# Kernel optimization log

Hardware: AMD Instinct MI355X
Metric: run time of the kernel (lower is better)

The kernel has to match this reference:

```python
import jax, jax.numpy as jnp
import numpy as np

R = 2          # candidate_radius
TEMP = 0.1     # temperature
MIN_E = 3
MAX_E = 8      # max_edges_per_node
EPS = 1e-6


def _neighbors(H, W, r):
    # grid neighbor indices (N,K) and relative positions (K,2), clamped at borders
    ys, xs = np.meshgrid(np.arange(H), np.arange(W), indexing='ij')
    idx_grid = ys * W + xs
    nbrs, rel = [], []
    for dy in range(-r, r + 1):
        for dx in range(-r, r + 1):
            if dy == 0 and dx == 0:
                continue
            ny = np.clip(ys + dy, 0, H - 1)
            nx = np.clip(xs + dx, 0, W - 1)
            nbrs.append(idx_grid[ny, nx].ravel())
            rel.append([dx / r, dy / r])
    return jnp.asarray(np.stack(nbrs, 1)), jnp.asarray(np.array(rel, np.float32))


def setup_inputs() -> dict:
    key = jax.random.key(0)
    ks = jax.random.split(key, 12)
    B, C, H, W = 2, 64, 128, 128
    hid = 64
    ein = 2 * C + 2  # edge scorer input dim
    s = 0.05
    return {
        'x':  jax.random.normal(ks[0], (B, C, H, W), jnp.float32),
        'W1': jax.random.normal(ks[1], (hid, ein), jnp.float32) * s,
        'b1': jnp.zeros((hid,), jnp.float32),
        'W2': jax.random.normal(ks[2], (hid // 2, hid), jnp.float32) * s,
        'b2': jnp.zeros((hid // 2,), jnp.float32),
        'W3': jax.random.normal(ks[3], (1, hid // 2), jnp.float32) * s,
        'b3': jnp.zeros((1,), jnp.float32),
        'thr': jnp.asarray(0.0, jnp.float32),
        'Wm': jax.random.normal(ks[4], (C, C), jnp.float32) * s,
        'bm': jnp.zeros((C,), jnp.float32),
        'Wo': jax.random.normal(ks[5], (C, C), jnp.float32) * s,
        'bo': jnp.zeros((C,), jnp.float32),
    }


def reference(x, W1, b1, W2, b2, W3, b3, thr, Wm, bm, Wo, bo):
    B, C, H, W = x.shape
    N = H * W
    nbr, rel = _neighbors(H, W, R)          # (N,K), (K,2)
    K = nbr.shape[1]

    nodes = x.transpose(0, 2, 3, 1).reshape(B, N, C)   # (B,N,C)
    h_tgt = jnp.take(nodes, nbr, axis=1)               # (B,N,K,C) gather neighbors

    # edge scorer layer1: split W1 over [h_src | h_tgt | rel_pos] to avoid (B,N,K,2C+2) concat
    z_src = nodes @ W1[:, :C].T                        # (B,N,hid)
    z_tgt = h_tgt @ W1[:, C:2 * C].T                   # (B,N,K,hid)
    z_pos = rel @ W1[:, 2 * C:].T                      # (K,hid)
    h1 = jax.nn.relu(z_src[:, :, None, :] + z_tgt + z_pos[None, None] + b1)
    h2 = jax.nn.relu(h1 @ W2.T + b2)
    edge_scores = jax.nn.sigmoid((h2 @ W3.T + b3)[..., 0])   # (B,N,K)

    thr_v = jax.nn.sigmoid(thr)
    keep_prob = jax.nn.sigmoid((edge_scores - thr_v) / TEMP)
    mask_thr = edge_scores >= thr_v
    counts = mask_thr.sum(axis=2)                       # (B,N)

    def topk_mask(k):
        _, idx = jax.lax.top_k(edge_scores, k)          # (B,N,k)
        return jax.nn.one_hot(idx, K, dtype=jnp.float32).sum(-2) > 0

    m_max = topk_mask(min(MAX_E, K))
    m_min = topk_mask(min(MIN_E, K))
    use_max = (counts > MAX_E)[..., None]
    use_min = (counts < MIN_E)[..., None]
    use_t = ~use_max & ~use_min
    final_mask = (use_max & m_max) | (use_min & m_min) | (use_t & mask_thr)

    msgs = jax.nn.relu(h_tgt @ Wm.T + bm)               # (B,N,K,C)
    w = (edge_scores * keep_prob * final_mask.astype(edge_scores.dtype))[..., None]
    agg = (msgs * w).sum(axis=2) / (w.sum(axis=2) + EPS)  # (B,N,C)

    out = nodes + agg @ Wo.T + bo
    return out.reshape(B, H, W, C).transpose(0, 3, 1, 2)
```

## Files before the change

### kernel.cpp

```cpp
#include <hip/hip_runtime.h>
#include <hip/hip_bf16.h>
#include <math.h>

#define NNODES 16384
#define KE 24

typedef float f32x4 __attribute__((ext_vector_type(4)));
typedef unsigned u32x4 __attribute__((ext_vector_type(4)));
typedef __fp16 half2_t __attribute__((ext_vector_type(2)));
typedef _Float16 half8_t __attribute__((ext_vector_type(8)));

union fragcast { u32x4 u; half8_t h; half2_t h2[4]; };

__global__ __launch_bounds__(256) void precompute_k(
    const float* __restrict__ x, const float* __restrict__ W1,
    const float* __restrict__ Wm, const float* __restrict__ b1,
    const float* __restrict__ bm,
    float* __restrict__ zsrc, float* __restrict__ ztgt, float* __restrict__ msg,
    float* __restrict__ zpos)
{
    __shared__ fragcast fragA[64 * 17];
    __shared__ float otL[4][16 * 68];

    const int t = threadIdx.x;
    const int l = t & 63;
    const int lcol = l & 15;
    const int lgrp = l >> 4;
    const int w = t >> 6;
    const int mat = blockIdx.x >> 8;
    const int tile = blockIdx.x & 255;
    const int n0g = tile * 128;
    const int b = n0g >> 14;
    const int nl0 = n0g & (NNODES - 1);

    if (blockIdx.x == 0) {
        for (int idx = t; idx < KE * 64; idx += 256) {
            int k = idx >> 6, h = idx & 63;
            int kk = k + (k >= 12 ? 1 : 0);
            int q5 = (kk * 52) >> 8;
            int dy = q5 - 2, dx = kk - 5 * q5 - 2;
            zpos[idx] = W1[h * 130 + 128] * (dx * 0.5f)
                      + W1[h * 130 + 129] * (dy * 0.5f);
        }
    }

    {
        const int mt = w;
        const int h = mt * 16 + lcol;
        const float* wrow = (mat == 0) ? (W1 + (size_t)h * 130)
                          : (mat == 1) ? (W1 + (size_t)h * 130 + 64)
                                       : (Wm + (size_t)h * 64);
        #pragma unroll
        for (int kt = 0; kt < 2; ++kt) {
            const float* wr = wrow + kt * 32 + lgrp * 8;
            fragcast fh, fl;
            #pragma unroll
            for (int d = 0; d < 4; ++d) {
                float e0 = wr[2 * d] * 64.f;
                float e1 = wr[2 * d + 1] * 64.f;
                half2_t hh = __builtin_amdgcn_cvt_pkrtz(e0, e1);
                fh.h2[d] = hh;
                fl.h2[d] = __builtin_amdgcn_cvt_pkrtz(e0 - (float)hh[0],
                                                      e1 - (float)hh[1]);
            }
            fragA[l * 17 + mt * 4 + kt * 2 + 0] = fh;
            fragA[l * 17 + mt * 4 + kt * 2 + 1] = fl;
        }
    }
    __syncthreads();

    float bv[4][4];
    #pragma unroll
    for (int mt = 0; mt < 4; ++mt)
        #pragma unroll
        for (int q = 0; q < 4; ++q) {
            int h = mt * 16 + lgrp * 4 + q;
            bv[mt][q] = (mat == 0) ? b1[h] : (mat == 2) ? bm[h] : 0.f;
        }

    const fragcast* fa = &fragA[l * 17];
    const float* xb = x + (size_t)b * 64 * NNODES + nl0;
    float* dst = (mat == 0) ? zsrc : (mat == 1) ? ztgt : msg;
    float* ot = &otL[w][0];

    #pragma unroll 1
    for (int nt = 0; nt < 2; ++nt) {
        const int nloc = w * 32 + nt * 16;

        fragcast Bh[2], Bl[2];
        #pragma unroll
        for (int kt = 0; kt < 2; ++kt) {
            const float* xc = xb + (size_t)(kt * 32 + lgrp * 8) * NNODES + nloc + lcol;
            float xv[8];
            #pragma unroll
            for (int i = 0; i < 8; ++i) xv[i] = xc[(size_t)i * NNODES];
            #pragma unroll
            for (int d = 0; d < 4; ++d) {
                half2_t hh = __builtin_amdgcn_cvt_pkrtz(xv[2 * d], xv[2 * d + 1]);
                Bh[kt].h2[d] = hh;
                Bl[kt].h2[d] = __builtin_amdgcn_cvt_pkrtz(xv[2 * d] - (float)hh[0],
                                                          xv[2 * d + 1] - (float)hh[1]);
            }
        }

        #pragma unroll
        for (int mt = 0; mt < 4; ++mt) {
            f32x4 acc = {0.f, 0.f, 0.f, 0.f};
            #pragma unroll
            for (int kt = 0; kt < 2; ++kt) {
                fragcast Ah = fa[mt * 4 + kt * 2 + 0];
                fragcast Al = fa[mt * 4 + kt * 2 + 1];
                acc = __builtin_amdgcn_mfma_f32_16x16x32_f16(Ah.h, Bh[kt].h, acc, 0, 0, 0);
                acc = __builtin_amdgcn_mfma_f32_16x16x32_f16(Al.h, Bh[kt].h, acc, 0, 0, 0);
                acc = __builtin_amdgcn_mfma_f32_16x16x32_f16(Ah.h, Bl[kt].h, acc, 0, 0, 0);
            }
            #pragma unroll
            for (int q = 0; q < 4; ++q) {
                float v = fmaf(acc[q], 0.015625f, bv[mt][q]);
                if (mat == 2) v = fmaxf(v, 0.f);
                ot[lcol * 68 + mt * 16 + lgrp * 4 + q] = v;
            }
        }

        {
            int nn = l >> 2, qt = l & 3;
            float* gout = dst + (size_t)(n0g + nloc + nn) * 64 + qt * 16;
            #pragma unroll
            for (int j = 0; j < 4; ++j) {
                f32x4 vv = *(const f32x4*)&ot[nn * 68 + qt * 16 + j * 4];
                *(float4*)(gout + j * 4) = make_float4(vv[0], vv[1], vv[2], vv[3]);
            }
        }
    }
}

__global__ __launch_bounds__(256, 1) void score_k(
    const float* __restrict__ zsrc, const float* __restrict__ ztgt,
    const float* __restrict__ zpos, const float* __restrict__ W2,
    const float* __restrict__ b2, const float* __restrict__ W3,
    const float* __restrict__ b3, float* __restrict__ scores)
{
    __shared__ fragcast fraglds[64 * 13];
    __shared__ float zpl[24 * 68];

    const int t = threadIdx.x;
    const int l = t & 63;
    const int lcol = l & 15;
    const int lgrp = l >> 4;
    const int w = t >> 6;
    const int wave = blockIdx.x * 4 + w;

    #pragma unroll
    for (int r = 0; r < 6; ++r) {
        int idx = r * 256 + t;
        zpl[(idx >> 6) * 68 + (idx & 63)] = zpos[idx];
    }
    {
        const int jt = w >> 1, kt = w & 1;
        fragcast fh, fl;
        const float* wr = W2 + (size_t)(jt * 16 + lcol) * 64 + kt * 32 + lgrp * 8;
        #pragma unroll
        for (int d = 0; d < 4; ++d) {
            float e0 = wr[2 * d] * 64.f;
            float e1 = wr[2 * d + 1] * 64.f;
            half2_t hh = __builtin_amdgcn_cvt_pkrtz(e0, e1);
            float r0 = e0 - (float)hh[0];
            float r1 = e1 - (float)hh[1];
            fh.h2[d] = hh;
            fl.h2[d] = __builtin_amdgcn_cvt_pkrtz(r0, r1);
        }
        fraglds[l * 13 + 0 + jt * 2 + kt] = fh;
        fraglds[l * 13 + 4 + jt * 2 + kt] = fl;
    }
    __syncthreads();

    const fragcast* fb = &fraglds[l * 13];
    const f32x4 b2l0 = *(const f32x4*)(b2 + lgrp * 4);
    const f32x4 b2l1 = *(const f32x4*)(b2 + 16 + lgrp * 4);
    const f32x4 w3l0 = *(const f32x4*)(W3 + lgrp * 4);
    const f32x4 w3l1 = *(const f32x4*)(W3 + 16 + lgrp * 4);
    const float b3s = b3[0];

    const int node0 = wave * 2;

    int kArr[3];
    float4 zsv[3][4], ztv[3][4];
    #pragma unroll
    for (int Mt = 0; Mt < 3; ++Mt) {
        const int ke = Mt * 16 + lcol;
        const int nsel = (ke >= 24) ? 1 : 0;
        const int node = node0 + nsel;
        const int k = ke - 24 * nsel;
        const int bb = node >> 14;
        const int nl = node & (NNODES - 1);
        const int yy = nl >> 7, xx = nl & 127;
        const int kk = k + (k >= 12 ? 1 : 0);
        const int q5 = (kk * 52) >> 8;
        const int dy = q5 - 2, dx = kk - 5 * q5 - 2;
        const int ny = min(max(yy + dy, 0), 127);
        const int nx = min(max(xx + dx, 0), 127);
        const int nbn = (bb << 14) + (ny << 7) + nx;
        kArr[Mt] = k;
        const float* zs = zsrc + (size_t)node * 64 + lgrp * 8;
        const float* zt = ztgt + (size_t)nbn * 64 + lgrp * 8;
        zsv[Mt][0] = *(const float4*)(zs);
        zsv[Mt][1] = *(const float4*)(zs + 4);
        zsv[Mt][2] = *(const float4*)(zs + 32);
        zsv[Mt][3] = *(const float4*)(zs + 36);
        ztv[Mt][0] = *(const float4*)(zt);
        ztv[Mt][1] = *(const float4*)(zt + 4);
        ztv[Mt][2] = *(const float4*)(zt + 32);
        ztv[Mt][3] = *(const float4*)(zt + 36);
    }

    #pragma unroll
    for (int Mt = 0; Mt < 3; ++Mt) {
        const float* zp = &zpl[kArr[Mt] * 68 + lgrp * 8];

        f32x4 ac0A = {0.f,0.f,0.f,0.f}, ac0B = {0.f,0.f,0.f,0.f};
        f32x4 ac1A = {0.f,0.f,0.f,0.f}, ac1B = {0.f,0.f,0.f,0.f};

        #pragma unroll
        for (int kt = 0; kt < 2; ++kt) {
            float4 a0 = zsv[Mt][2 * kt], a1 = zsv[Mt][2 * kt + 1];
            float4 t0 = ztv[Mt][2 * kt], t1 = ztv[Mt][2 * kt + 1];
            float4 p0 = *(const float4*)(zp + kt * 32);
            float4 p1 = *(const float4*)(zp + kt * 32 + 4);
            float v[8];
            v[0] = fmaxf(a0.x + t0.x + p0.x, 0.f);
            v[1] = fmaxf(a0.y + t0.y + p0.y, 0.f);
            v[2] = fmaxf(a0.z + t0.z + p0.z, 0.f);
            v[3] = fmaxf(a0.w + t0.w + p0.w, 0.f);
            v[4] = fmaxf(a1.x + t1.x + p1.x, 0.f);
            v[5] = fmaxf(a1.y + t1.y + p1.y, 0.f);
            v[6] = fmaxf(a1.z + t1.z + p1.z, 0.f);
            v[7] = fmaxf(a1.w + t1.w + p1.w, 0.f);

            fragcast Bh, Bl;
            #pragma unroll
            for (int d = 0; d < 4; ++d) {
                float e0 = v[2 * d], e1 = v[2 * d + 1];
                half2_t hh = __builtin_amdgcn_cvt_pkrtz(e0, e1);
                float r0 = e0 - (float)hh[0];
                float r1 = e1 - (float)hh[1];
                Bh.h2[d] = hh;
                Bl.h2[d] = __builtin_amdgcn_cvt_pkrtz(r0, r1);
            }

            ac0A = __builtin_amdgcn_mfma_f32_16x16x32_f16(fb[0 + kt].h, Bh.h, ac0A, 0, 0, 0);
            ac1A = __builtin_amdgcn_mfma_f32_16x16x32_f16(fb[2 + kt].h, Bh.h, ac1A, 0, 0, 0);
            ac0B = __builtin_amdgcn_mfma_f32_16x16x32_f16(fb[4 + kt].h, Bh.h, ac0B, 0, 0, 0);
            ac1B = __builtin_amdgcn_mfma_f32_16x16x32_f16(fb[6 + kt].h, Bh.h, ac1B, 0, 0, 0);
            ac0B = __builtin_amdgcn_mfma_f32_16x16x32_f16(fb[0 + kt].h, Bl.h, ac0B, 0, 0, 0);
            ac1B = __builtin_amdgcn_mfma_f32_16x16x32_f16(fb[2 + kt].h, Bl.h, ac1B, 0, 0, 0);
        }

        const f32x4 s0 = ac0A + ac0B;
        const f32x4 s1 = ac1A + ac1B;
        float sacc = 0.f;
        #pragma unroll
        for (int q = 0; q < 4; ++q) {
            sacc = fmaf(fmaxf(fmaf(s0[q], 0.015625f, b2l0[q]), 0.f), w3l0[q], sacc);
            sacc = fmaf(fmaxf(fmaf(s1[q], 0.015625f, b2l1[q]), 0.f), w3l1[q], sacc);
        }
        sacc += __shfl_xor(sacc, 16);
        sacc += __shfl_xor(sacc, 32);
        float sig = 1.f / (1.f + expf(-(sacc + b3s)));
        if (l < 16)
            scores[(size_t)node0 * 24 + Mt * 16 + l] = sig;
    }
}

__global__ __launch_bounds__(256) void agg_k(
    const float* __restrict__ x, const float* __restrict__ scores,
    const float* __restrict__ msg, const float* __restrict__ Wo,
    const float* __restrict__ bo, const float* __restrict__ thrp,
    float* __restrict__ out)
{
    __shared__ float sc[768];
    __shared__ float wl[768];
    __shared__ float sumw[32];
    __shared__ float aggL[32][64];
    __shared__ float ot[64][33];

    const int t = threadIdx.x;
    const int n0 = blockIdx.x * 32;
    const int b = n0 >> 14;
    const int nl0 = n0 & (NNODES - 1);
    const float thr_v = 1.f / (1.f + expf(-thrp[0]));

    #pragma unroll
    for (int rep = 0; rep < 3; ++rep)
        sc[rep * 256 + t] = scores[(size_t)n0 * 24 + rep * 256 + t];
    __syncthreads();

    #pragma unroll
    for (int rep = 0; rep < 3; ++rep) {
        int e = rep * 256 + t;
        int nl = (int)(((unsigned)(e >> 3) * 171u) >> 9);
        int k = e - nl * 24;
        float s_e = sc[e];
        int rank = 0, cnt = 0;
        #pragma unroll
        for (int j = 0; j < 24; ++j) {
            float sj = sc[nl * 24 + j];
            rank += (sj > s_e || (sj == s_e && j < k)) ? 1 : 0;
            cnt  += (sj >= thr_v) ? 1 : 0;
        }
        bool mask = (cnt > 8) ? (rank < 8)
                  : ((cnt < 3) ? (rank < 3) : (s_e >= thr_v));
        float keep = 1.f / (1.f + expf(-(s_e - thr_v) * 10.f));
        wl[e] = mask ? s_e * keep : 0.f;
    }
    __syncthreads();

    if (t < 32) {
        float s = 0.f;
        #pragma unroll
        for (int k = 0; k < 24; ++k) s += wl[t * 24 + k];
        sumw[t] = s + 1e-6f;
    }
    __syncthreads();

    const int lane = t & 63;
    const int g4 = t >> 6;

    #pragma unroll
    for (int it = 0; it < 8; ++it) {
        int nl = g4 + it * 4;
        int nn = nl0 + nl;
        int yy = nn >> 7, xx = nn & 127;
        float acc = 0.f;
        #pragma unroll
        for (int k = 0; k < 24; ++k) {
            int kk = k + (k >= 12 ? 1 : 0);
            int q5 = (kk * 52) >> 8;
            int dy = q5 - 2, dx = kk - 5 * q5 - 2;
            int ny = min(max(yy + dy, 0), 127);
            int nx = min(max(xx + dx, 0), 127);
            int nb = (b << 14) + (ny << 7) + nx;
            acc = fmaf(wl[nl * 24 + k], msg[(size_t)nb * 64 + lane], acc);
        }
        aggL[nl][lane] = acc / sumw[nl];
    }

    float4 wo[16];
    #pragma unroll
    for (int c4 = 0; c4 < 16; ++c4) wo[c4] = ((const float4*)Wo)[lane * 16 + c4];
    __syncthreads();

    #pragma unroll
    for (int it = 0; it < 8; ++it) {
        int nl = g4 + it * 4;
        const float4* ar = (const float4*)aggL[nl];
        float a0 = 0.f, a1 = 0.f, a2 = 0.f, a3 = 0.f;
        #pragma unroll
        for (int c4 = 0; c4 < 16; ++c4) {
            float4 wv = wo[c4];
            float4 av = ar[c4];
            a0 = fmaf(av.x, wv.x, a0);
            a1 = fmaf(av.y, wv.y, a1);
            a2 = fmaf(av.z, wv.z, a2);
            a3 = fmaf(av.w, wv.w, a3);
        }
        float v = (a0 + a1) + (a2 + a3) + bo[lane]
                + x[(size_t)b * 64 * NNODES + (size_t)lane * NNODES + nl0 + nl];
        ot[lane][nl] = v;
    }
    __syncthreads();

    #pragma unroll
    for (int rep = 0; rep < 2; ++rep) {
        int idx = rep * 256 + t;
        int o = idx >> 3, p = idx & 7;
        float4 v = make_float4(ot[o][4 * p + 0], ot[o][4 * p + 1],
                               ot[o][4 * p + 2], ot[o][4 * p + 3]);
        *(float4*)(out + (size_t)b * 64 * NNODES + (size_t)o * NNODES + nl0 + 4 * p) = v;
    }
}

extern "C" void kernel_launch(void* const* d_in, const int* in_sizes, int n_in,
                              void* d_out, int out_size, void* d_ws, size_t ws_size,
                              hipStream_t stream)
{
    const float* x   = (const float*)d_in[0];
    const float* W1  = (const float*)d_in[1];
    const float* b1  = (const float*)d_in[2];
    const float* W2  = (const float*)d_in[3];
    const float* b2  = (const float*)d_in[4];
    const float* W3  = (const float*)d_in[5];
    const float* b3  = (const float*)d_in[6];
    const float* thr = (const float*)d_in[7];
    const float* Wm  = (const float*)d_in[8];
    const float* bm  = (const float*)d_in[9];
    const float* Wo  = (const float*)d_in[10];
    const float* bo  = (const float*)d_in[11];
    float* out = (float*)d_out;
    float* ws  = (float*)d_ws;

    float* zsrc   = ws;
    float* ztgt   = ws + 2097152;
    float* msg    = ws + 4194304;
    float* scores = ws + 6291456;
    float* zpos   = ws + 7077888;

    hipLaunchKernelGGL(precompute_k, dim3(768), dim3(256), 0, stream,
                       x, W1, Wm, b1, bm, zsrc, ztgt, msg, zpos);
    hipLaunchKernelGGL(score_k, dim3(4096), dim3(256), 0, stream,
                       zsrc, ztgt, zpos, W2, b2, W3, b3, scores);
    hipLaunchKernelGGL(agg_k, dim3(1024), dim3(256), 0, stream,
                       x, scores, msg, Wo, bo, thr, out);
}
```

Before: 84.92 us.

## Stage 5x20 message window in LDS for aggregation with 16-node blocks

```diff
diff --git a/kernel.cpp b/kernel.cpp
--- a/kernel.cpp
+++ b/kernel.cpp
@@ -277,105 +277,116 @@
     const float* __restrict__ bo, const float* __restrict__ thrp,
     float* __restrict__ out)
 {
-    __shared__ float sc[768];
-    __shared__ float wl[768];
-    __shared__ float sumw[32];
-    __shared__ float aggL[32][64];
-    __shared__ float ot[64][33];
+    __shared__ float mwin[100 * 64];
+    __shared__ float sc[384];
+    __shared__ float wle[384];
+    __shared__ float sumw[16];
+    __shared__ float aggL[16][64];
+    __shared__ float ot[16 * 68];
 
     const int t = threadIdx.x;
-    const int n0 = blockIdx.x * 32;
-    const int b = n0 >> 14;
-    const int nl0 = n0 & (NNODES - 1);
+    const int blkbase = blockIdx.x * 16;
+    const int b = blkbase >> 14;
+    const int y = (blkbase >> 7) & 127;
+    const int x0 = blkbase & 127;
+    const int nl0 = blkbase & (NNODES - 1);
     const float thr_v = 1.f / (1.f + expf(-thrp[0]));
 
-    #pragma unroll
-    for (int rep = 0; rep < 3; ++rep)
-        sc[rep * 256 + t] = scores[(size_t)n0 * 24 + rep * 256 + t];
-    __syncthreads();
-
-    #pragma unroll
-    for (int rep = 0; rep < 3; ++rep) {
+    for (int i = t; i < 1600; i += 256) {
+        int row = i >> 4, f4 = i & 15;
+        int wy = (row * 3277) >> 16;
+        int cx = row - wy * 20;
+        int gy = min(max(y + wy - 2, 0), 127);
+        int gx = min(max(x0 + cx - 2, 0), 127);
+        int gn = (b << 14) + (gy << 7) + gx;
+        *(float4*)&mwin[row * 64 + f4 * 4] =
+            *(const float4*)(msg + (size_t)gn * 64 + f4 * 4);
+    }
+    #pragma unroll
+    for (int rep = 0; rep < 2; ++rep) {
         int e = rep * 256 + t;
-        int nl = (int)(((unsigned)(e >> 3) * 171u) >> 9);
-        int k = e - nl * 24;
-        float s_e = sc[e];
-        int rank = 0, cnt = 0;
-        #pragma unroll
-        for (int j = 0; j < 24; ++j) {
-            float sj = sc[nl * 24 + j];
-            rank += (sj > s_e || (sj == s_e && j < k)) ? 1 : 0;
-            cnt  += (sj >= thr_v) ? 1 : 0;
-        }
-        bool mask = (cnt > 8) ? (rank < 8)
-                  : ((cnt < 3) ? (rank < 3) : (s_e >= thr_v));
-        float keep = 1.f / (1.f + expf(-(s_e - thr_v) * 10.f));
-        wl[e] = mask ? s_e * keep : 0.f;
-    }
-    __syncthreads();
-
-    if (t < 32) {
+        if (e < 384) sc[e] = scores[(size_t)blkbase * 24 + e];
+    }
+    __syncthreads();
+
+    #pragma unroll
+    for (int rep = 0; rep < 2; ++rep) {
+        int e = rep * 256 + t;
+        if (e < 384) {
+            int nl = (int)(((unsigned)(e >> 3) * 171u) >> 9);
+            int k = e - nl * 24;
+            float s_e = sc[e];
+            int rank = 0, cnt = 0;
+            #pragma unroll
+            for (int j = 0; j < 24; ++j) {
+                float sj = sc[nl * 24 + j];
+                rank += (sj > s_e || (sj == s_e && j < k)) ? 1 : 0;
+                cnt  += (sj >= thr_v) ? 1 : 0;
+            }
+            bool mask = (cnt > 8) ? (rank < 8)
+                      : ((cnt < 3) ? (rank < 3) : (s_e >= thr_v));
+            float keep = 1.f / (1.f + expf(-(s_e - thr_v) * 10.f));
+            wle[e] = mask ? s_e * keep : 0.f;
+        }
+    }
+    __syncthreads();
+
+    if (t < 16) {
         float s = 0.f;
         #pragma unroll
-        for (int k = 0; k < 24; ++k) s += wl[t * 24 + k];
+        for (int k = 0; k < 24; ++k) s += wle[t * 24 + k];
         sumw[t] = s + 1e-6f;
     }
     __syncthreads();
 
-    const int lane = t & 63;
-    const int g4 = t >> 6;
-
-    #pragma unroll
-    for (int it = 0; it < 8; ++it) {
-        int nl = g4 + it * 4;
-        int nn = nl0 + nl;
-        int yy = nn >> 7, xx = nn & 127;
-        float acc = 0.f;
-        #pragma unroll
-        for (int k = 0; k < 24; ++k) {
-            int kk = k + (k >= 12 ? 1 : 0);
-            int q5 = (kk * 52) >> 8;
-            int dy = q5 - 2, dx = kk - 5 * q5 - 2;
-            int ny = min(max(yy + dy, 0), 127);
-            int nx = min(max(xx + dx, 0), 127);
-            int nb = (b << 14) + (ny << 7) + nx;
-            acc = fmaf(wl[nl * 24 + k], msg[(size_t)nb * 64 + lane], acc);
-        }
-        aggL[nl][lane] = acc / sumw[nl];
-    }
-
-    float4 wo[16];
-    #pragma unroll
-    for (int c4 = 0; c4 < 16; ++c4) wo[c4] = ((const float4*)Wo)[lane * 16 + c4];
-    __syncthreads();
-
-    #pragma unroll
-    for (int it = 0; it < 8; ++it) {
-        int nl = g4 + it * 4;
-        const float4* ar = (const float4*)aggL[nl];
-        float a0 = 0.f, a1 = 0.f, a2 = 0.f, a3 = 0.f;
-        #pragma unroll
-        for (int c4 = 0; c4 < 16; ++c4) {
-            float4 wv = wo[c4];
-            float4 av = ar[c4];
-            a0 = fmaf(av.x, wv.x, a0);
-            a1 = fmaf(av.y, wv.y, a1);
-            a2 = fmaf(av.z, wv.z, a2);
-            a3 = fmaf(av.w, wv.w, a3);
-        }
-        float v = (a0 + a1) + (a2 + a3) + bo[lane]
-                + x[(size_t)b * 64 * NNODES + (size_t)lane * NNODES + nl0 + nl];
-        ot[lane][nl] = v;
-    }
-    __syncthreads();
-
-    #pragma unroll
-    for (int rep = 0; rep < 2; ++rep) {
-        int idx = rep * 256 + t;
-        int o = idx >> 3, p = idx & 7;
-        float4 v = make_float4(ot[o][4 * p + 0], ot[o][4 * p + 1],
-                               ot[o][4 * p + 2], ot[o][4 * p + 3]);
-        *(float4*)(out + (size_t)b * 64 * NNODES + (size_t)o * NNODES + nl0 + 4 * p) = v;
+    {
+        const int c = t & 63, w = t >> 6;
+        #pragma unroll
+        for (int it = 0; it < 4; ++it) {
+            int nl = w * 4 + it;
+            float acc = 0.f;
+            #pragma unroll
+            for (int k = 0; k < 24; ++k) {
+                int kk = k + (k >= 12 ? 1 : 0);
+                int q5 = (kk * 52) >> 8;
+                int dy = q5 - 2, dx = kk - 5 * q5 - 2;
+                int row = (dy + 2) * 20 + nl + dx + 2;
+                acc = fmaf(wle[nl * 24 + k], mwin[row * 64 + c], acc);
+            }
+            aggL[nl][c] = acc / sumw[nl];
+        }
+    }
+    __syncthreads();
+
+    {
+        const int o = t & 63, g4 = t >> 6;
+        const float4* wr = (const float4*)(Wo + (size_t)o * 64);
+        #pragma unroll
+        for (int it = 0; it < 4; ++it) {
+            int nl = g4 + it * 4;
+            const float4* ar = (const float4*)aggL[nl];
+            float a0 = 0.f, a1 = 0.f, a2 = 0.f, a3 = 0.f;
+            #pragma unroll
+            for (int c4 = 0; c4 < 16; ++c4) {
+                float4 wv = wr[c4];
+                float4 av = ar[c4];
+                a0 = fmaf(av.x, wv.x, a0);
+                a1 = fmaf(av.y, wv.y, a1);
+                a2 = fmaf(av.z, wv.z, a2);
+                a3 = fmaf(av.w, wv.w, a3);
+            }
+            float v = (a0 + a1) + (a2 + a3) + bo[o]
+                    + x[(size_t)b * 64 * NNODES + (size_t)o * NNODES + nl0 + nl];
+            ot[nl * 68 + o] = v;
+        }
+    }
+    __syncthreads();
+
+    {
+        int o = t >> 2, jj = t & 3;
+        float4 v = make_float4(ot[(4 * jj + 0) * 68 + o], ot[(4 * jj + 1) * 68 + o],
+                               ot[(4 * jj + 2) * 68 + o], ot[(4 * jj + 3) * 68 + o]);
+        *(float4*)(out + (size_t)b * 64 * NNODES + (size_t)o * NNODES + nl0 + 4 * jj) = v;
     }
 }
 
@@ -408,6 +419,6 @@
                        x, W1, Wm, b1, bm, zsrc, ztgt, msg, zpos);
     hipLaunchKernelGGL(score_k, dim3(4096), dim3(256), 0, stream,
                        zsrc, ztgt, zpos, W2, b2, W3, b3, scores);
-    hipLaunchKernelGGL(agg_k, dim3(1024), dim3(256), 0, stream,
+    hipLaunchKernelGGL(agg_k, dim3(2048), dim3(256), 0, stream,
                        x, scores, msg, Wo, bo, thr, out);
 }
```

Result: slower. 185.7 us (+118.7%).
